# Kernel tuning notes

Measured on AMD Instinct MI355X. Metric: run time of the kernel, lower is better.

Reference implementation:

```python
import jax, jax.numpy as jnp
import numpy as np

N_NODES = 100000
N_EDGES = 1200000
D = 64
EPS = 1e-7
BETA = 1.0


def setup_inputs() -> dict:
    key = jax.random.key(0)
    k1, k2, k3, k4, k5 = jax.random.split(key, 5)
    node_feats = jax.random.normal(k1, (N_NODES, D), dtype=jnp.float32)
    edge_feats = jax.random.normal(k2, (N_EDGES, D), dtype=jnp.float32)
    W = jax.random.normal(k3, (D, D), dtype=jnp.float32) * (1.0 / np.sqrt(D))
    b = jnp.zeros((D,), dtype=jnp.float32)
    scale = jnp.ones((1,), dtype=jnp.float32)
    src = jax.random.randint(k4, (N_EDGES,), 0, N_NODES, dtype=jnp.int32)
    dst = jnp.sort(jax.random.randint(k5, (N_EDGES,), 0, N_NODES, dtype=jnp.int32))
    return {"node_feats": node_feats, "edge_feats": edge_feats, "W": W, "b": b,
            "scale": scale, "src": src, "dst": dst}


def reference(node_feats, edge_feats, W, b, scale, src, dst):
    # u_add_e: message = h[src] + edge_feats, then relu + eps  -> [E, D]
    m = jax.nn.relu(node_feats[src] + edge_feats) + EPS
    z = m * BETA
    # edge_softmax: per-destination, per-channel softmax over incoming edges
    mx = jax.ops.segment_max(z, dst, num_segments=N_NODES)      # [N, D]
    mx = jnp.where(jnp.isfinite(mx), mx, 0.0)                   # zero-degree guard
    e = jnp.exp(z - mx[dst])
    denom = jax.ops.segment_sum(e, dst, num_segments=N_NODES)   # [N, D]
    a = e / denom[dst]
    # weighted scatter-sum aggregation
    agg = jax.ops.segment_sum(m * a, dst, num_segments=N_NODES)  # [N, D]
    # MessageNorm: l2-normalize msg, rescale by ||node_feats||_2 * scale
    msg = agg / jnp.maximum(jnp.linalg.norm(agg, axis=-1, keepdims=True), 1e-12)
    feats_norm = jnp.linalg.norm(node_feats, axis=-1, keepdims=True)
    msg = msg * feats_norm * scale
    feats = node_feats + msg
    # mlp_layers=1 -> single Linear
    return feats @ W.T + b
```

## Files before the change

### kernel.cpp

```cpp
#include <hip/hip_runtime.h>

#define NN 100000
#define NE 1200000
#define DD 64
#define EPSV 1e-7f

__global__ __launch_bounds__(256)
void build_offsets(const int* __restrict__ dst, int* __restrict__ off) {
    int i = blockIdx.x * 256 + threadIdx.x;
    if (i >= NE) return;
    int d = dst[i];
    int prev = (i == 0) ? -1 : dst[i - 1];
    for (int n = prev + 1; n <= d; ++n) off[n] = i;
    if (i == NE - 1) {
        for (int n = d + 1; n <= NN; ++n) off[n] = NE;
    }
}

__global__ __launch_bounds__(256, 4)
void genconv_kernel(const float* __restrict__ node_feats,
                    const float* __restrict__ edge_feats,
                    const float* __restrict__ W,
                    const float* __restrict__ b,
                    const float* __restrict__ scale,
                    const int* __restrict__ src,
                    const int* __restrict__ dst,
                    const int* __restrict__ off,
                    float* __restrict__ out)
{
    __shared__ float Wt[64 * 65];
    __shared__ float featL[4 * 64];
    const int tid = threadIdx.x;
    for (int idx = tid; idx < 64 * 64; idx += 256) {
        int j = idx >> 6, d = idx & 63;
        Wt[d * 65 + j] = W[idx];
    }
    __syncthreads();

    const int wave = tid >> 6;
    const int lane = tid & 63;
    const int n = blockIdx.x * 4 + wave;
    if (n >= NN) return;

    int e_start, e_end;
    if (off) {
        e_start = off[n];
        e_end   = off[n + 1];
    } else {
        int target = (lane < 32) ? n : (n + 1);
        int lo = 0, hi = NE;
        while (lo < hi) {
            int mid = (lo + hi) >> 1;
            if (dst[mid] < target) lo = mid + 1; else hi = mid;
        }
        e_start = __shfl(lo, 0, 64);
        e_end   = __shfl(lo, 32, 64);
    }

    const int eg = lane >> 4;
    const int cg = lane & 15;
    const float4* nf4 = (const float4*)node_feats;
    const float4* ef4 = (const float4*)edge_feats;

    float4 ssum = {0.f, 0.f, 0.f, 0.f};
    float4 wsum = {0.f, 0.f, 0.f, 0.f};
    float* sp = (float*)&ssum;
    float* wp = (float*)&wsum;
    for (int base = e_start; base < e_end; base += 8) {
        #pragma unroll
        for (int u = 0; u < 2; ++u) {
            const int i  = base + u * 4 + eg;
            const bool ok = i < e_end;
            const int ic = ok ? i : (e_end - 1);
            const int sk = src[ic];
            float4 ef = ef4[(size_t)ic * 16 + cg];
            float4 nf = nf4[(size_t)sk * 16 + cg];
            const float* ep = (const float*)&ef;
            const float* np = (const float*)&nf;
            #pragma unroll
            for (int t = 0; t < 4; ++t) {
                float v = fmaxf(np[t] + ep[t], 0.f) + EPSV;
                float e = ok ? __expf(v) : 0.f;
                sp[t] += e;
                wp[t] += e * v;
            }
        }
    }
    float4 agg;
    float* ap = (float*)&agg;
    #pragma unroll
    for (int t = 0; t < 4; ++t) {
        sp[t] += __shfl_xor(sp[t], 16, 64);
        sp[t] += __shfl_xor(sp[t], 32, 64);
        wp[t] += __shfl_xor(wp[t], 16, 64);
        wp[t] += __shfl_xor(wp[t], 32, 64);
        ap[t] = (sp[t] > 0.f) ? (wp[t] / sp[t]) : 0.f;
    }

    float4 h4 = nf4[(size_t)n * 16 + cg];
    float* hp = (float*)&h4;
    float a2 = ap[0]*ap[0] + ap[1]*ap[1] + ap[2]*ap[2] + ap[3]*ap[3];
    float h2 = hp[0]*hp[0] + hp[1]*hp[1] + hp[2]*hp[2] + hp[3]*hp[3];
    #pragma unroll
    for (int o = 8; o >= 1; o >>= 1) {
        a2 += __shfl_xor(a2, o, 64);
        h2 += __shfl_xor(h2, o, 64);
    }
    float k = sqrtf(h2) * scale[0] / fmaxf(sqrtf(a2), 1e-12f);
    float4 feat;
    float* fp = (float*)&feat;
    #pragma unroll
    for (int t = 0; t < 4; ++t) fp[t] = hp[t] + ap[t] * k;

    if (eg == 0) *(float4*)&featL[wave * 64 + cg * 4] = feat;
    float acc = b[lane];
    #pragma unroll
    for (int c4 = 0; c4 < 16; ++c4) {
        float4 f = *(const float4*)&featL[wave * 64 + c4 * 4];
        const float* fq = (const float*)&f;
        #pragma unroll
        for (int t = 0; t < 4; ++t)
            acc = fmaf(fq[t], Wt[(c4 * 4 + t) * 65 + lane], acc);
    }
    out[(size_t)n * DD + lane] = acc;
}

extern "C" void kernel_launch(void* const* d_in, const int* in_sizes, int n_in,
                              void* d_out, int out_size, void* d_ws, size_t ws_size,
                              hipStream_t stream) {
    const float* node_feats = (const float*)d_in[0];
    const float* edge_feats = (const float*)d_in[1];
    const float* W          = (const float*)d_in[2];
    const float* b          = (const float*)d_in[3];
    const float* scale      = (const float*)d_in[4];
    const int*   src        = (const int*)d_in[5];
    const int*   dst        = (const int*)d_in[6];
    float*       out        = (float*)d_out;

    int* off = nullptr;
    if (ws_size >= (size_t)(NN + 1) * sizeof(int)) {
        off = (int*)d_ws;
        build_offsets<<<(NE + 255) / 256, 256, 0, stream>>>(dst, off);
    }
    const int blocks = (NN + 3) / 4;
    genconv_kernel<<<blocks, 256, 0, stream>>>(node_feats, edge_feats, W, b,
                                               scale, src, dst, off, out);
}
```

Baseline: 479.4 us.

## Overlap W staging with gather, peel first 16 edges, use nontemporal loads/stores

Moves the __syncthreads after the edge aggregation so the shared-memory W transpose load overlaps with the gather phase. Peels the first 16 edges into a batch that issues all src/edge loads before the node gathers, which raises memory-level parallelism for the typical degree of about 12. Edge features and outputs use nontemporal loads and stores to avoid polluting cache that the reused node_feats gathers rely on. The extra unrolled batch adds register pressure and code size.

```diff
diff --git a/kernel.cpp b/kernel.cpp
--- a/kernel.cpp
+++ b/kernel.cpp
@@ -4,6 +4,8 @@
 #define NE 1200000
 #define DD 64
 #define EPSV 1e-7f
+
+typedef float nfloat4 __attribute__((ext_vector_type(4)));
 
 __global__ __launch_bounds__(256)
 void build_offsets(const int* __restrict__ dst, int* __restrict__ off) {
@@ -31,98 +33,151 @@
     __shared__ float Wt[64 * 65];
     __shared__ float featL[4 * 64];
     const int tid = threadIdx.x;
-    for (int idx = tid; idx < 64 * 64; idx += 256) {
+
+    #pragma unroll
+    for (int r = 0; r < 16; ++r) {
+        int idx = r * 256 + tid;
         int j = idx >> 6, d = idx & 63;
         Wt[d * 65 + j] = W[idx];
     }
-    __syncthreads();
 
     const int wave = tid >> 6;
     const int lane = tid & 63;
     const int n = blockIdx.x * 4 + wave;
-    if (n >= NN) return;
-
-    int e_start, e_end;
-    if (off) {
-        e_start = off[n];
-        e_end   = off[n + 1];
-    } else {
-        int target = (lane < 32) ? n : (n + 1);
-        int lo = 0, hi = NE;
-        while (lo < hi) {
-            int mid = (lo + hi) >> 1;
-            if (dst[mid] < target) lo = mid + 1; else hi = mid;
-        }
-        e_start = __shfl(lo, 0, 64);
-        e_end   = __shfl(lo, 32, 64);
-    }
+    const bool active = (n < NN);
 
     const int eg = lane >> 4;
     const int cg = lane & 15;
-    const float4* nf4 = (const float4*)node_feats;
-    const float4* ef4 = (const float4*)edge_feats;
-
-    float4 ssum = {0.f, 0.f, 0.f, 0.f};
-    float4 wsum = {0.f, 0.f, 0.f, 0.f};
-    float* sp = (float*)&ssum;
-    float* wp = (float*)&wsum;
-    for (int base = e_start; base < e_end; base += 8) {
-        #pragma unroll
-        for (int u = 0; u < 2; ++u) {
-            const int i  = base + u * 4 + eg;
-            const bool ok = i < e_end;
-            const int ic = ok ? i : (e_end - 1);
-            const int sk = src[ic];
-            float4 ef = ef4[(size_t)ic * 16 + cg];
-            float4 nf = nf4[(size_t)sk * 16 + cg];
-            const float* ep = (const float*)&ef;
-            const float* np = (const float*)&nf;
-            #pragma unroll
-            for (int t = 0; t < 4; ++t) {
-                float v = fmaxf(np[t] + ep[t], 0.f) + EPSV;
-                float e = ok ? __expf(v) : 0.f;
-                sp[t] += e;
-                wp[t] += e * v;
-            }
-        }
-    }
-    float4 agg;
-    float* ap = (float*)&agg;
-    #pragma unroll
-    for (int t = 0; t < 4; ++t) {
-        sp[t] += __shfl_xor(sp[t], 16, 64);
-        sp[t] += __shfl_xor(sp[t], 32, 64);
-        wp[t] += __shfl_xor(wp[t], 16, 64);
-        wp[t] += __shfl_xor(wp[t], 32, 64);
-        ap[t] = (sp[t] > 0.f) ? (wp[t] / sp[t]) : 0.f;
-    }
-
-    float4 h4 = nf4[(size_t)n * 16 + cg];
-    float* hp = (float*)&h4;
-    float a2 = ap[0]*ap[0] + ap[1]*ap[1] + ap[2]*ap[2] + ap[3]*ap[3];
-    float h2 = hp[0]*hp[0] + hp[1]*hp[1] + hp[2]*hp[2] + hp[3]*hp[3];
-    #pragma unroll
-    for (int o = 8; o >= 1; o >>= 1) {
-        a2 += __shfl_xor(a2, o, 64);
-        h2 += __shfl_xor(h2, o, 64);
-    }
-    float k = sqrtf(h2) * scale[0] / fmaxf(sqrtf(a2), 1e-12f);
-    float4 feat;
-    float* fp = (float*)&feat;
-    #pragma unroll
-    for (int t = 0; t < 4; ++t) fp[t] = hp[t] + ap[t] * k;
-
-    if (eg == 0) *(float4*)&featL[wave * 64 + cg * 4] = feat;
+    const float4*  nf4 = (const float4*)node_feats;
+    const nfloat4* ef4 = (const nfloat4*)edge_feats;
+
     float acc = b[lane];
-    #pragma unroll
-    for (int c4 = 0; c4 < 16; ++c4) {
-        float4 f = *(const float4*)&featL[wave * 64 + c4 * 4];
-        const float* fq = (const float*)&f;
-        #pragma unroll
-        for (int t = 0; t < 4; ++t)
-            acc = fmaf(fq[t], Wt[(c4 * 4 + t) * 65 + lane], acc);
-    }
-    out[(size_t)n * DD + lane] = acc;
+
+    if (active) {
+        int e_start, e_end;
+        if (off) {
+            e_start = off[n];
+            e_end   = off[n + 1];
+        } else {
+            int target = (lane < 32) ? n : (n + 1);
+            int lo = 0, hi = NE;
+            while (lo < hi) {
+                int mid = (lo + hi) >> 1;
+                if (dst[mid] < target) lo = mid + 1; else hi = mid;
+            }
+            e_start = __shfl(lo, 0, 64);
+            e_end   = __shfl(lo, 32, 64);
+        }
+
+        float4 h4 = nf4[(size_t)n * 16 + cg];
+
+        float4 ssum = {0.f, 0.f, 0.f, 0.f};
+        float4 wsum = {0.f, 0.f, 0.f, 0.f};
+        float* sp = (float*)&ssum;
+        float* wp = (float*)&wsum;
+        const int deg = e_end - e_start;
+
+        if (deg > 0) {
+            int     sk[4];
+            nfloat4 efv[4];
+            bool    okv[4];
+            #pragma unroll
+            for (int u = 0; u < 4; ++u) {
+                int i = e_start + u * 4 + eg;
+                bool ok = i < e_end;
+                okv[u] = ok;
+                int ic = ok ? i : e_start;
+                sk[u]  = src[ic];
+                efv[u] = __builtin_nontemporal_load(&ef4[(size_t)ic * 16 + cg]);
+            }
+            float4 nfv[4];
+            #pragma unroll
+            for (int u = 0; u < 4; ++u)
+                nfv[u] = nf4[(size_t)sk[u] * 16 + cg];
+            #pragma unroll
+            for (int u = 0; u < 4; ++u) {
+                const float* np = (const float*)&nfv[u];
+                #pragma unroll
+                for (int t = 0; t < 4; ++t) {
+                    float v = fmaxf(np[t] + efv[u][t], 0.f) + EPSV;
+                    float e = okv[u] ? __expf(v) : 0.f;
+                    sp[t] += e;
+                    wp[t] += e * v;
+                }
+            }
+            for (int base = e_start + 16; base < e_end; base += 8) {
+                int     sk2[2];
+                nfloat4 ef2[2];
+                bool    ok2[2];
+                #pragma unroll
+                for (int u = 0; u < 2; ++u) {
+                    int i = base + u * 4 + eg;
+                    bool ok = i < e_end;
+                    ok2[u] = ok;
+                    int ic = ok ? i : base;
+                    sk2[u] = src[ic];
+                    ef2[u] = __builtin_nontemporal_load(&ef4[(size_t)ic * 16 + cg]);
+                }
+                float4 nf2[2];
+                #pragma unroll
+                for (int u = 0; u < 2; ++u)
+                    nf2[u] = nf4[(size_t)sk2[u] * 16 + cg];
+                #pragma unroll
+                for (int u = 0; u < 2; ++u) {
+                    const float* np = (const float*)&nf2[u];
+                    #pragma unroll
+                    for (int t = 0; t < 4; ++t) {
+                        float v = fmaxf(np[t] + ef2[u][t], 0.f) + EPSV;
+                        float e = ok2[u] ? __expf(v) : 0.f;
+                        sp[t] += e;
+                        wp[t] += e * v;
+                    }
+                }
+            }
+        }
+
+        float4 agg;
+        float* ap = (float*)&agg;
+        #pragma unroll
+        for (int t = 0; t < 4; ++t) {
+            sp[t] += __shfl_xor(sp[t], 16, 64);
+            sp[t] += __shfl_xor(sp[t], 32, 64);
+            wp[t] += __shfl_xor(wp[t], 16, 64);
+            wp[t] += __shfl_xor(wp[t], 32, 64);
+            ap[t] = (sp[t] > 0.f) ? (wp[t] / sp[t]) : 0.f;
+        }
+
+        float* hp = (float*)&h4;
+        float a2 = ap[0]*ap[0] + ap[1]*ap[1] + ap[2]*ap[2] + ap[3]*ap[3];
+        float h2 = hp[0]*hp[0] + hp[1]*hp[1] + hp[2]*hp[2] + hp[3]*hp[3];
+        #pragma unroll
+        for (int o = 8; o >= 1; o >>= 1) {
+            a2 += __shfl_xor(a2, o, 64);
+            h2 += __shfl_xor(h2, o, 64);
+        }
+        float k = sqrtf(h2) * scale[0] / fmaxf(sqrtf(a2), 1e-12f);
+
+        float4 feat;
+        float* fp = (float*)&feat;
+        #pragma unroll
+        for (int t = 0; t < 4; ++t) fp[t] = hp[t] + ap[t] * k;
+
+        if (eg == 0) *(float4*)&featL[wave * 64 + cg * 4] = feat;
+    }
+
+    __syncthreads();
+
+    if (active) {
+        #pragma unroll
+        for (int c4 = 0; c4 < 16; ++c4) {
+            float4 f = *(const float4*)&featL[wave * 64 + c4 * 4];
+            const float* fq = (const float*)&f;
+            #pragma unroll
+            for (int t = 0; t < 4; ++t)
+                acc = fmaf(fq[t], Wt[(c4 * 4 + t) * 65 + lane], acc);
+        }
+        __builtin_nontemporal_store(acc, &out[(size_t)n * DD + lane]);
+    }
 }
 
 extern "C" void kernel_launch(void* const* d_in, const int* in_sizes, int n_in,
```

Measured after the change: 455.9 us. 1.05x faster.
